# Optimization experiments

Hardware: AMD Instinct MI355X
Metric: run time of the kernel (lower is better)

Reference implementation:

```python
import jax, jax.numpy as jnp
import numpy as np
from jax import lax

SEGMENTS = 64
KERNEL = 5


def setup_inputs() -> dict:
    key = jax.random.key(0)
    k1, k2, k3 = jax.random.split(key, 3)
    B, S, F = 4, 4096, 1024
    A6 = 512 * 6
    inp = jax.random.normal(k1, (B, S, F), dtype=jnp.float32)
    W = jax.random.normal(k2, (A6, F), dtype=jnp.float32) * (1.0 / np.sqrt(F))
    b = jax.random.normal(k3, (A6,), dtype=jnp.float32) * 0.01
    return {"inp": inp, "W": W, "b": b}


def reference(inp, W, b):
    # Fused projection: [B,S,F] @ [F,6A] -> [B,S,6A]
    x = jnp.einsum('bsf,af->bsa', inp, W) + b
    qry, key, val, seg, loc, out = jnp.split(x, 6, axis=2)  # each [B,S,A]
    B, S, A = out.shape

    # Global aggregated attention branch
    agg = qry.mean(axis=1)                              # [B,A]
    scores = jnp.einsum('ba,bsa->bs', agg, key)         # [B,S]
    w = jax.nn.softmax(scores, axis=1)                  # [B,S]
    ctx = jnp.einsum('bs,bsa->ba', w, val)              # [B,A]
    aggregated = ctx[:, None, :] * out                  # [B,S,A]

    # Segment max-pool branch
    nseg = S // SEGMENTS
    seg4 = seg.reshape(B, nseg, SEGMENTS, A)
    seg_max = seg4.max(axis=2, keepdims=True)           # [B,nseg,1,A]
    segment_max_pooled = (seg_max * out.reshape(B, nseg, SEGMENTS, A)).reshape(B, S, A)

    # Local sliding-window max-pool branch (stride 1, pad KERNEL//2, -inf padding)
    pad = KERNEL // 2
    local_max_pooled = lax.reduce_window(
        loc, -jnp.inf, lax.max,
        window_dimensions=(1, KERNEL, 1),
        window_strides=(1, 1, 1),
        padding=((0, 0), (pad, pad), (0, 0)))           # [B,S,A]

    return aggregated + segment_max_pooled + local_max_pooled
```

## Files before the change

kernel.cpp:

```cpp
#include <hip/hip_runtime.h>
#include <hip/hip_bf16.h>
#include <stdint.h>

#define B_    4
#define S_    4096
#define F_    1024
#define A_    512
#define N3_   1536
#define M_    16384

#define BM    256
#define BK    64
#define NT    (F_ / BK)
#define LDP   266

typedef __attribute__((ext_vector_type(8))) __bf16 bf16x8;

#define MFMA(a, b, c) __builtin_amdgcn_mfma_f32_16x16x32_bf16((a), (b), (c), 0, 0, 0)
typedef __attribute__((ext_vector_type(4))) float f32x4;

__device__ __forceinline__ float bflo(unsigned int u) {
  union { unsigned int i; float f; } v; v.i = u << 16; return v.f;
}
__device__ __forceinline__ float bfhi(unsigned int u) {
  union { unsigned int i; float f; } v; v.i = u & 0xffff0000u; return v.f;
}
__device__ __forceinline__ float bf1(unsigned short u) {
  union { unsigned int i; float f; } v; v.i = ((unsigned int)u) << 16; return v.f;
}
__device__ __forceinline__ unsigned short bfc(float f) {
  return __builtin_bit_cast(unsigned short, __float2bfloat16(f));
}
__device__ __forceinline__ ushort4 cvt_bf4(float4 v) {
  ushort4 o;
  o.x = bfc(v.x); o.y = bfc(v.y); o.z = bfc(v.z); o.w = bfc(v.w);
  return o;
}

typedef __attribute__((address_space(3))) unsigned int lds_uint;
typedef const __attribute__((address_space(1))) unsigned int glob_uint;
__device__ __forceinline__ void lds_load16(const void* g, void* l) {
  __builtin_amdgcn_global_load_lds((glob_uint*)g, (lds_uint*)l, 16, 0, 0);
}

__global__ __launch_bounds__(256) void convert_mean_kernel(
    const float* __restrict__ inp, const float* __restrict__ W,
    unsigned short* __restrict__ inp_bf, unsigned short* __restrict__ w_bf,
    float* __restrict__ mu) {
  int blk = blockIdx.x;
  int t   = threadIdx.x;
  int r0  = blk * 32;
  int b   = r0 >> 12;
  float acc0 = 0.f, acc1 = 0.f, acc2 = 0.f, acc3 = 0.f;
  for (int r = 0; r < 32; r++) {
    size_t row = (size_t)(r0 + r);
    float4 v = ((const float4*)(inp + row * F_))[t];
    acc0 += v.x; acc1 += v.y; acc2 += v.z; acc3 += v.w;
    ((ushort4*)(inp_bf + row * F_))[t] = cvt_bf4(v);
  }
  atomicAdd(&mu[b * F_ + t * 4 + 0], acc0);
  atomicAdd(&mu[b * F_ + t * 4 + 1], acc1);
  atomicAdd(&mu[b * F_ + t * 4 + 2], acc2);
  atomicAdd(&mu[b * F_ + t * 4 + 3], acc3);

  const float* Wc = W + (size_t)N3_ * F_;
  const int n4 = (N3_ * F_) / 4;
  for (int i = blk * 256 + t; i < n4; i += 512 * 256) {
    ((ushort4*)w_bf)[i] = cvt_bf4(((const float4*)Wc)[i]);
  }
}

__global__ void agg_kernel(const float* __restrict__ mu, const float* __restrict__ W,
                           const float* __restrict__ bias, float* __restrict__ agg) {
  int gw = blockIdx.x * 4 + (threadIdx.x >> 6);
  int lane = threadIdx.x & 63;
  int b = gw >> 9, a = gw & 511;
  const float4* wr = (const float4*)(W + (size_t)a * F_);
  const float4* mr = (const float4*)(mu + b * F_);
  float s = 0.f;
#pragma unroll
  for (int k = 0; k < 4; k++) {
    float4 wv = wr[lane + 64 * k], mv = mr[lane + 64 * k];
    s += wv.x * mv.x + wv.y * mv.y + wv.z * mv.z + wv.w * mv.w;
  }
  for (int off = 32; off; off >>= 1) s += __shfl_down(s, off);
  if (lane == 0) agg[b * A_ + a] = s * (1.f / S_) + bias[a];
}

__global__ void v_kernel(const float* __restrict__ agg, const float* __restrict__ W,
                         float* __restrict__ v) {
  int fc = blockIdx.x;
  int ac = blockIdx.y;
  int t = threadIdx.x;
  int f = fc * 256 + t;
  const float* Wk = W + (size_t)A_ * F_;
  float s0 = 0.f, s1 = 0.f, s2 = 0.f, s3 = 0.f;
  int a0 = ac * 64;
  for (int a = a0; a < a0 + 64; a++) {
    float wv = Wk[(size_t)a * F_ + f];
    s0 += agg[a] * wv;
    s1 += agg[A_ + a] * wv;
    s2 += agg[2 * A_ + a] * wv;
    s3 += agg[3 * A_ + a] * wv;
  }
  atomicAdd(&v[f], s0);
  atomicAdd(&v[F_ + f], s1);
  atomicAdd(&v[2 * F_ + f], s2);
  atomicAdd(&v[3 * F_ + f], s3);
}

__global__ __launch_bounds__(256) void scores_u_kernel(
    const unsigned short* __restrict__ inp_bf, const float* __restrict__ v,
    float* __restrict__ uP, float* __restrict__ mlzl) {
  int blk = blockIdx.x;
  int b = blk >> 6, ch = blk & 63;
  int s0 = ch * 64;
  int t = threadIdx.x, lane = t & 63, wv = t >> 6;
  __shared__ float sc[64];
  __shared__ float wsl[64];

  const float4* vp = (const float4*)(v + b * F_);
  float4 va0 = vp[lane * 2], va1 = vp[lane * 2 + 1];
  float4 vb0 = vp[(lane + 64) * 2], vb1 = vp[(lane + 64) * 2 + 1];
#pragma unroll
  for (int i = 0; i < 16; i++) {
    int r = wv * 16 + i;
    const uint4* ip = (const uint4*)(inp_bf + ((size_t)(b * S_ + s0 + r)) * F_);
    uint4 x0 = ip[lane], x1 = ip[lane + 64];
    float s = bflo(x0.x) * va0.x + bfhi(x0.x) * va0.y + bflo(x0.y) * va0.z + bfhi(x0.y) * va0.w +
              bflo(x0.z) * va1.x + bfhi(x0.z) * va1.y + bflo(x0.w) * va1.z + bfhi(x0.w) * va1.w +
              bflo(x1.x) * vb0.x + bfhi(x1.x) * vb0.y + bflo(x1.y) * vb0.z + bfhi(x1.y) * vb0.w +
              bflo(x1.z) * vb1.x + bfhi(x1.z) * vb1.y + bflo(x1.w) * vb1.z + bfhi(x1.w) * vb1.w;
    for (int off = 32; off; off >>= 1) s += __shfl_down(s, off);
    if (lane == 0) sc[r] = s;
  }
  __syncthreads();

  float m = -1e30f;
#pragma unroll
  for (int i = 0; i < 64; i++) m = fmaxf(m, sc[i]);
  if (t < 64) wsl[t] = __expf(sc[t] - m);
  __syncthreads();

  {
    const unsigned short* xp = inp_bf + ((size_t)(b * S_ + s0)) * F_ + t * 4;
    float a0 = 0.f, a1 = 0.f, a2 = 0.f, a3 = 0.f;
    for (int s = 0; s < 64; s++) {
      uint2 xv = *(const uint2*)&xp[(size_t)s * F_];
      float w = wsl[s];
      a0 += w * bflo(xv.x); a1 += w * bfhi(xv.x);
      a2 += w * bflo(xv.y); a3 += w * bfhi(xv.y);
    }
    float4 o; o.x = a0; o.y = a1; o.z = a2; o.w = a3;
    *(float4*)&uP[(size_t)blk * 1024 + t * 4] = o;
  }
  if (t == 0) {
    float Z = 0.f;
#pragma unroll
    for (int i = 0; i < 64; i++) Z += wsl[i];
    mlzl[blk * 2] = m; mlzl[blk * 2 + 1] = Z;
  }
}

__global__ void ufin_kernel(const float* __restrict__ uP, const float* __restrict__ mlzl,
                            float* __restrict__ u) {
  int b = blockIdx.x >> 2, fs = blockIdx.x & 3;
  int f = fs * 256 + threadIdx.x;
  float M = -1e30f;
#pragma unroll
  for (int i = 0; i < 64; i++) M = fmaxf(M, mlzl[(b * 64 + i) * 2]);
  float Z = 0.f;
#pragma unroll
  for (int i = 0; i < 64; i++) Z += __expf(mlzl[(b * 64 + i) * 2] - M) * mlzl[(b * 64 + i) * 2 + 1];
  float acc = 0.f;
  for (int ch = 0; ch < 64; ch++) {
    float sc = __expf(mlzl[(b * 64 + ch) * 2] - M);
    acc += sc * uP[(size_t)(b * 64 + ch) * 1024 + f];
  }
  u[b * F_ + f] = acc / Z;
}

__global__ void ctx_kernel(const float* __restrict__ u, const float* __restrict__ W,
                           const float* __restrict__ bias, float* __restrict__ ctx) {
  int gw = blockIdx.x * 4 + (threadIdx.x >> 6);
  int lane = threadIdx.x & 63;
  int b = gw >> 9, a = gw & 511;
  const float4* wr = (const float4*)(W + (size_t)(2 * A_ + a) * F_);
  const float4* ur = (const float4*)(u + b * F_);
  float s = 0.f;
#pragma unroll
  for (int k = 0; k < 4; k++) {
    float4 wv = wr[lane + 64 * k], uv = ur[lane + 64 * k];
    s += wv.x * uv.x + wv.y * uv.y + wv.z * uv.z + wv.w * uv.w;
  }
  for (int off = 32; off; off >>= 1) s += __shfl_down(s, off);
  if (lane == 0) ctx[b * A_ + a] = s + bias[2 * A_ + a];
}

__global__ __launch_bounds__(512, 2) void gemm_fused(
    const __hip_bfloat16* __restrict__ Abf,
    const __hip_bfloat16* __restrict__ Wbf,
    const float* __restrict__ biasP,
    const float* __restrict__ ctx,
    float* __restrict__ out,
    unsigned short* __restrict__ sideLoc,
    float* __restrict__ sideGO) {
  extern __shared__ unsigned short smem[];
  unsigned short* ldsA = smem;
  unsigned short* ldsB = smem + 32768;
  unsigned short* Xt   = smem;
  float* segred = (float*)((char*)smem + 192 * LDP * 2);

  int bid = blockIdx.x;
  int swz = (bid & 7) * 64 + (bid >> 3);
  int mb = swz >> 3;
  int nb = swz & 7;

  int tid  = threadIdx.x;
  int lane = tid & 63;
  int wv   = tid >> 6;
  int wm   = wv >> 1;
  int wn   = wv & 1;
  int lo   = lane & 15, hi = lane >> 4, sw = lane & 7;

  int bir0 = (((hi * 16)      ^ (sw << 4)) >> 1);
  int bir1 = (((64 + hi * 16) ^ (sw << 4)) >> 1);

  const __hip_bfloat16* Ab = Abf + (size_t)mb * BM * F_;

  int srow = tid >> 3;
  int sel  = ((tid & 7) ^ (srow & 7)) * 8;
  int ldst = wv * 512;

  f32x4 acc[4][6];
#pragma unroll
  for (int i = 0; i < 4; i++)
#pragma unroll
    for (int j = 0; j < 6; j++) acc[i][j] = (f32x4){0.f, 0.f, 0.f, 0.f};

  int aBase = (wm * 64 + lo) * 64;
  int bBase = (wn * 96 + lo) * 64;

#define STG_A(kt_, buf_, r_)                                                              \
  lds_load16(Ab + (size_t)((r_) * 64 + srow) * F_ + (kt_) * BK + sel,                     \
             ldsA + (buf_) * 16384 + (r_) * 4096 + ldst)
#define STG_B(kt_, buf_, q_)                                                              \
  lds_load16(Wbf + (size_t)((q_) * 512 + nb * 64 + srow) * F_ + (kt_) * BK + sel,         \
             ldsB + (buf_) * 12288 + (q_) * 4096 + ldst)

  bf16x8 af[4][2], b01[2][2], b23[2][2], b45[2][2];

  STG_A(0, 0, 0); STG_A(0, 0, 1); STG_A(0, 0, 2); STG_A(0, 0, 3);
  STG_B(0, 0, 0); STG_B(0, 0, 1); STG_B(0, 0, 2);
  asm volatile("s_waitcnt vmcnt(0)" ::: "memory");
  __builtin_amdgcn_s_barrier();
#pragma unroll
  for (int i = 0; i < 4; i++) {
    af[i][0] = *(const bf16x8*)&ldsA[aBase + i * 1024 + bir0];
    af[i][1] = *(const bf16x8*)&ldsA[aBase + i * 1024 + bir1];
  }
#pragma unroll
  for (int j = 0; j < 2; j++) {
    b01[j][0] = *(const bf16x8*)&ldsB[bBase + j * 1024 + bir0];
    b01[j][1] = *(const bf16x8*)&ldsB[bBase + j * 1024 + bir1];
  }

  for (int kt = 0; kt < NT; ++kt) {
    int c = kt & 1, nx = c ^ 1;
    bool pf = (kt + 1 < NT);
    const unsigned short* lb  = ldsB + c * 12288;
    const unsigned short* lan = ldsA + nx * 16384;
    const unsigned short* lbn = ldsB + nx * 12288;

    if (pf) { STG_A(kt + 1, nx, 0); STG_A(kt + 1, nx, 1); STG_A(kt + 1, nx, 2); STG_A(kt + 1, nx, 3); }
    asm volatile("s_waitcnt lgkmcnt(0)" ::: "memory");
    __builtin_amdgcn_sched_barrier(0);
    __builtin_amdgcn_s_setprio(1);
#pragma unroll
    for (int i = 0; i < 4; i++)
#pragma unroll
      for (int j = 0; j < 2; j++) {
        acc[i][j] = MFMA(af[i][0], b01[j][0], acc[i][j]);
        acc[i][j] = MFMA(af[i][1], b01[j][1], acc[i][j]);
      }
    __builtin_amdgcn_s_setprio(0);
#pragma unroll
    for (int j = 0; j < 2; j++) {
      b23[j][0] = *(const bf16x8*)&lb[bBase + (2 + j) * 1024 + bir0];
      b23[j][1] = *(const bf16x8*)&lb[bBase + (2 + j) * 1024 + bir1];
    }
    __builtin_amdgcn_s_barrier();

    if (pf) { STG_B(kt + 1, nx, 0); STG_B(kt + 1, nx, 1); STG_B(kt + 1, nx, 2); }
    asm volatile("s_waitcnt lgkmcnt(0)" ::: "memory");
    __builtin_amdgcn_sched_barrier(0);
    __builtin_amdgcn_s_setprio(1);
#pragma unroll
    for (int i = 0; i < 4; i++)
#pragma unroll
      for (int j = 0; j < 2; j++) {
        acc[i][2 + j] = MFMA(af[i][0], b23[j][0], acc[i][2 + j]);
        acc[i][2 + j] = MFMA(af[i][1], b23[j][1], acc[i][2 + j]);
      }
    __builtin_amdgcn_s_setprio(0);
#pragma unroll
    for (int j = 0; j < 2; j++) {
      b45[j][0] = *(const bf16x8*)&lb[bBase + (4 + j) * 1024 + bir0];
      b45[j][1] = *(const bf16x8*)&lb[bBase + (4 + j) * 1024 + bir1];
    }
    __builtin_amdgcn_s_barrier();

    asm volatile("s_waitcnt lgkmcnt(0)" ::: "memory");
    __builtin_amdgcn_sched_barrier(0);
    __builtin_amdgcn_s_setprio(1);
#pragma unroll
    for (int i = 0; i < 4; i++)
#pragma unroll
      for (int j = 0; j < 2; j++) {
        acc[i][4 + j] = MFMA(af[i][0], b45[j][0], acc[i][4 + j]);
        acc[i][4 + j] = MFMA(af[i][1], b45[j][1], acc[i][4 + j]);
      }
    __builtin_amdgcn_s_setprio(0);
    if (pf) asm volatile("s_waitcnt vmcnt(0)" ::: "memory");
    __builtin_amdgcn_s_barrier();
    if (pf) {
#pragma unroll
      for (int i = 0; i < 4; i++) {
        af[i][0] = *(const bf16x8*)&lan[aBase + i * 1024 + bir0];
        af[i][1] = *(const bf16x8*)&lan[aBase + i * 1024 + bir1];
      }
#pragma unroll
      for (int j = 0; j < 2; j++) {
        b01[j][0] = *(const bf16x8*)&lbn[bBase + j * 1024 + bir0];
        b01[j][1] = *(const bf16x8*)&lbn[bBase + j * 1024 + bir1];
      }
    }
  }
#undef STG_A
#undef STG_B

  float bias_r[6];
#pragma unroll
  for (int fj = 0; fj < 6; fj++) {
    int cl = wn * 96 + fj * 16 + lo;
    bias_r[fj] = biasP[(cl >> 6) * 512 + nb * 64 + (cl & 63)];
  }
#pragma unroll
  for (int fi = 0; fi < 4; fi++) {
#pragma unroll
    for (int fj = 0; fj < 6; fj++) {
      int cl = wn * 96 + fj * 16 + lo;
      int r  = wm * 64 + fi * 16 + hi * 4;
      float v0 = acc[fi][fj][0] + bias_r[fj];
      float v1 = acc[fi][fj][1] + bias_r[fj];
      float v2 = acc[fi][fj][2] + bias_r[fj];
      float v3 = acc[fi][fj][3] + bias_r[fj];
      unsigned int u01 = (unsigned int)bfc(v0) | ((unsigned int)bfc(v1) << 16);
      unsigned int u23 = (unsigned int)bfc(v2) | ((unsigned int)bfc(v3) << 16);
      *(unsigned int*)&Xt[cl * LDP + r]     = u01;
      *(unsigned int*)&Xt[cl * LDP + r + 2] = u23;
    }
  }
  __syncthreads();

  if (tid < 256) {
    int seg = tid >> 6, c = tid & 63;
    int base = c * LDP + seg * 64;
    float m = -1e30f;
#pragma unroll
    for (int k = 0; k < 32; k++) {
      unsigned int uu = *(const unsigned int*)&Xt[base + 2 * k];
      m = fmaxf(m, fmaxf(bflo(uu), bfhi(uu)));
    }
    segred[seg * 64 + c] = m;
  }
  __syncthreads();

  {
    int c  = lane;
    int r0 = wv * 32;
    int b  = mb >> 4;
    int gcol = nb * 64 + c;
    float g = ctx[b * 512 + gcol] + segred[(r0 >> 6) * 64 + c];
    int lbase = (64 + c) * LDP;
    int obase = (128 + c) * LDP;
    float lw0 = bf1(Xt[lbase + max(r0 - 2, 0)]);
    float lw1 = bf1(Xt[lbase + max(r0 - 1, 0)]);
    float lw2 = bf1(Xt[lbase + r0]);
    float lw3 = bf1(Xt[lbase + r0 + 1]);
    size_t obase_g = ((size_t)(mb * 256 + r0)) * 512 + gcol;
#pragma unroll
    for (int j = 0; j < 32; j++) {
      int rn = min(r0 + j + 2, 255);
      float lw4 = bf1(Xt[lbase + rn]);
      float lm = fmaxf(fmaxf(fmaxf(lw0, lw1), fmaxf(lw2, lw3)), lw4);
      float o = bf1(Xt[obase + r0 + j]);
      out[obase_g + (size_t)j * 512] = g * o + lm;
      lw0 = lw1; lw1 = lw2; lw2 = lw3; lw3 = lw4;
    }
  }

  if (tid < 256) {
    int rsel = tid >> 6, c = tid & 63;
    int r = (rsel < 2) ? rsel : (252 + rsel);
    int b = mb >> 4;
    float g = ctx[b * 512 + nb * 64 + c] + segred[(r >> 6) * 64 + c];
    float o = bf1(Xt[(128 + c) * LDP + r]);
    int gr = mb * 4 + rsel;
    sideLoc[gr * 512 + nb * 64 + c] = Xt[(64 + c) * LDP + r];
    sideGO[gr * 512 + nb * 64 + c]  = g * o;
  }
}

__global__ void fixup_kernel(const unsigned short* __restrict__ sideLoc,
                             const float* __restrict__ sideGO,
                             float* __restrict__ out) {
  int rb = blockIdx.x;
  int tb = rb & 15;
  int t = threadIdx.x;
  int rsel = t >> 6, cq = t & 63;
#pragma unroll
  for (int k = 0; k < 8; k++) {
    int c = cq * 8 + k;
    float miss;
    int rl;
    if (rsel == 0) {
      if (tb == 0) continue;
      miss = fmaxf(bf1(sideLoc[((rb - 1) * 4 + 2) * 512 + c]),
                   bf1(sideLoc[((rb - 1) * 4 + 3) * 512 + c]));
      rl = 0;
    } else if (rsel == 1) {
      if (tb == 0) continue;
      miss = bf1(sideLoc[((rb - 1) * 4 + 3) * 512 + c]);
      rl = 1;
    } else if (rsel == 2) {
      if (tb == 15) continue;
      miss = bf1(sideLoc[((rb + 1) * 4 + 0) * 512 + c]);
      rl = 254;
    } else {
      if (tb == 15) continue;
      miss = fmaxf(bf1(sideLoc[((rb + 1) * 4 + 0) * 512 + c]),
                   bf1(sideLoc[((rb + 1) * 4 + 1) * 512 + c]));
      rl = 255;
    }
    size_t oi = ((size_t)rb * 256 + rl) * 512 + c;
    float cand = sideGO[(rb * 4 + rsel) * 512 + c] + miss;
    out[oi] = fmaxf(out[oi], cand);
  }
}

extern "C" void kernel_launch(void* const* d_in, const int* in_sizes, int n_in,
                              void* d_out, int out_size, void* d_ws, size_t ws_size,
                              hipStream_t stream) {
  const float* inp  = (const float*)d_in[0];
  const float* W    = (const float*)d_in[1];
  const float* bias = (const float*)d_in[2];
  float* out = (float*)d_out;
  char* ws = (char*)d_ws;

  const size_t INP_OFF  = 0;
  const size_t W_OFF    = 33554432;
  const size_t MU_OFF   = 36700160;
  const size_t U_OFF    = MU_OFF + 16384;
  const size_t V_OFF    = U_OFF + 16384;
  const size_t AGG_OFF  = V_OFF + 16384;
  const size_t CTX_OFF  = AGG_OFF + 8192;
  const size_t SL_OFF   = CTX_OFF + 8192;
  const size_t SG_OFF   = SL_OFF + 262144;
  const size_t UP_OFF   = SG_OFF + 524288;
  const size_t ML_OFF   = UP_OFF + 1048576;

  unsigned short* inp_bf = (unsigned short*)(ws + INP_OFF);
  unsigned short* w_bf   = (unsigned short*)(ws + W_OFF);
  float* mu     = (float*)(ws + MU_OFF);
  float* u      = (float*)(ws + U_OFF);
  float* v      = (float*)(ws + V_OFF);
  float* agg    = (float*)(ws + AGG_OFF);
  float* ctx    = (float*)(ws + CTX_OFF);
  unsigned short* sideLoc = (unsigned short*)(ws + SL_OFF);
  float* sideGO = (float*)(ws + SG_OFF);
  float* uP     = (float*)(ws + UP_OFF);
  float* mlzl   = (float*)(ws + ML_OFF);

  hipFuncSetAttribute(reinterpret_cast<const void*>(gemm_fused),
                      hipFuncAttributeMaxDynamicSharedMemorySize, 114688);

  hipMemsetAsync(ws + MU_OFF, 0, 3 * 16384, stream);
  convert_mean_kernel<<<512, 256, 0, stream>>>(inp, W, inp_bf, w_bf, mu);
  agg_kernel<<<512, 256, 0, stream>>>(mu, W, bias, agg);
  v_kernel<<<dim3(4, 8), 256, 0, stream>>>(agg, W, v);
  scores_u_kernel<<<256, 256, 0, stream>>>(inp_bf, v, uP, mlzl);
  ufin_kernel<<<16, 256, 0, stream>>>(uP, mlzl, u);
  ctx_kernel<<<512, 256, 0, stream>>>(u, W, bias, ctx);
  gemm_fused<<<512, 512, 114688, stream>>>((const __hip_bfloat16*)inp_bf,
                                           (const __hip_bfloat16*)w_bf,
                                           bias + 3 * A_, ctx, out, sideLoc, sideGO);
  fixup_kernel<<<64, 256, 0, stream>>>(sideLoc, sideGO, out);
}
```

Baseline: 128.2 us.

## Restructure GEMM main loop to issue all next-tile loads up front with partial vmcnt wait

Changes the double-buffered GEMM K-loop so that each iteration first issues all global-to-LDS loads for the next A and B tiles. It then waits with vmcnt(7) so only the current tile's loads must be complete, and reads the fragments from the current buffer. The old schedule interleaved A and B prefetch with barriers between MFMA phases and preloaded the next fragments at the end of each iteration. The aim is fewer barriers per iteration and longer overlap of global loads with MFMA work. In exchange, the per-iteration LDS fragment loads now sit on the critical path before the first MFMA group, and the explicit lgkmcnt waits and sched_barriers are gone.

```diff
diff --git a/kernel.cpp b/kernel.cpp
--- a/kernel.cpp
+++ b/kernel.cpp
@@ -15,9 +15,9 @@
 #define LDP   266
 
 typedef __attribute__((ext_vector_type(8))) __bf16 bf16x8;
+typedef __attribute__((ext_vector_type(4))) float f32x4;
 
 #define MFMA(a, b, c) __builtin_amdgcn_mfma_f32_16x16x32_bf16((a), (b), (c), 0, 0, 0)
-typedef __attribute__((ext_vector_type(4))) float f32x4;
 
 __device__ __forceinline__ float bflo(unsigned int u) {
   union { unsigned int i; float f; } v; v.i = u << 16; return v.f;
@@ -248,33 +248,36 @@
   lds_load16(Wbf + (size_t)((q_) * 512 + nb * 64 + srow) * F_ + (kt_) * BK + sel,         \
              ldsB + (buf_) * 12288 + (q_) * 4096 + ldst)
 
-  bf16x8 af[4][2], b01[2][2], b23[2][2], b45[2][2];
-
   STG_A(0, 0, 0); STG_A(0, 0, 1); STG_A(0, 0, 2); STG_A(0, 0, 3);
   STG_B(0, 0, 0); STG_B(0, 0, 1); STG_B(0, 0, 2);
-  asm volatile("s_waitcnt vmcnt(0)" ::: "memory");
-  __builtin_amdgcn_s_barrier();
-#pragma unroll
-  for (int i = 0; i < 4; i++) {
-    af[i][0] = *(const bf16x8*)&ldsA[aBase + i * 1024 + bir0];
-    af[i][1] = *(const bf16x8*)&ldsA[aBase + i * 1024 + bir1];
-  }
-#pragma unroll
-  for (int j = 0; j < 2; j++) {
-    b01[j][0] = *(const bf16x8*)&ldsB[bBase + j * 1024 + bir0];
-    b01[j][1] = *(const bf16x8*)&ldsB[bBase + j * 1024 + bir1];
-  }
 
   for (int kt = 0; kt < NT; ++kt) {
     int c = kt & 1, nx = c ^ 1;
     bool pf = (kt + 1 < NT);
-    const unsigned short* lb  = ldsB + c * 12288;
-    const unsigned short* lan = ldsA + nx * 16384;
-    const unsigned short* lbn = ldsB + nx * 12288;
-
-    if (pf) { STG_A(kt + 1, nx, 0); STG_A(kt + 1, nx, 1); STG_A(kt + 1, nx, 2); STG_A(kt + 1, nx, 3); }
-    asm volatile("s_waitcnt lgkmcnt(0)" ::: "memory");
-    __builtin_amdgcn_sched_barrier(0);
+    const unsigned short* la = ldsA + c * 16384;
+    const unsigned short* lb = ldsB + c * 12288;
+
+    __builtin_amdgcn_s_barrier();
+    if (pf) {
+      STG_A(kt + 1, nx, 0); STG_A(kt + 1, nx, 1); STG_A(kt + 1, nx, 2); STG_A(kt + 1, nx, 3);
+      STG_B(kt + 1, nx, 0); STG_B(kt + 1, nx, 1); STG_B(kt + 1, nx, 2);
+      asm volatile("s_waitcnt vmcnt(7)" ::: "memory");
+    } else {
+      asm volatile("s_waitcnt vmcnt(0)" ::: "memory");
+    }
+    __builtin_amdgcn_s_barrier();
+
+    bf16x8 af[4][2], b01[2][2], b23[2][2], b45[2][2];
+#pragma unroll
+    for (int i = 0; i < 4; i++) {
+      af[i][0] = *(const bf16x8*)&la[aBase + i * 1024 + bir0];
+      af[i][1] = *(const bf16x8*)&la[aBase + i * 1024 + bir1];
+    }
+#pragma unroll
+    for (int j = 0; j < 2; j++) {
+      b01[j][0] = *(const bf16x8*)&lb[bBase + j * 1024 + bir0];
+      b01[j][1] = *(const bf16x8*)&lb[bBase + j * 1024 + bir1];
+    }
     __builtin_amdgcn_s_setprio(1);
 #pragma unroll
     for (int i = 0; i < 4; i++)
@@ -284,16 +287,12 @@
         acc[i][j] = MFMA(af[i][1], b01[j][1], acc[i][j]);
       }
     __builtin_amdgcn_s_setprio(0);
+
 #pragma unroll
     for (int j = 0; j < 2; j++) {
       b23[j][0] = *(const bf16x8*)&lb[bBase + (2 + j) * 1024 + bir0];
       b23[j][1] = *(const bf16x8*)&lb[bBase + (2 + j) * 1024 + bir1];
     }
-    __builtin_amdgcn_s_barrier();
-
-    if (pf) { STG_B(kt + 1, nx, 0); STG_B(kt + 1, nx, 1); STG_B(kt + 1, nx, 2); }
-    asm volatile("s_waitcnt lgkmcnt(0)" ::: "memory");
-    __builtin_amdgcn_sched_barrier(0);
     __builtin_amdgcn_s_setprio(1);
 #pragma unroll
     for (int i = 0; i < 4; i++)
@@ -303,15 +302,12 @@
         acc[i][2 + j] = MFMA(af[i][1], b23[j][1], acc[i][2 + j]);
       }
     __builtin_amdgcn_s_setprio(0);
+
 #pragma unroll
     for (int j = 0; j < 2; j++) {
       b45[j][0] = *(const bf16x8*)&lb[bBase + (4 + j) * 1024 + bir0];
       b45[j][1] = *(const bf16x8*)&lb[bBase + (4 + j) * 1024 + bir1];
     }
-    __builtin_amdgcn_s_barrier();
-
-    asm volatile("s_waitcnt lgkmcnt(0)" ::: "memory");
-    __builtin_amdgcn_sched_barrier(0);
     __builtin_amdgcn_s_setprio(1);
 #pragma unroll
     for (int i = 0; i < 4; i++)
@@ -321,23 +317,11 @@
         acc[i][4 + j] = MFMA(af[i][1], b45[j][1], acc[i][4 + j]);
       }
     __builtin_amdgcn_s_setprio(0);
-    if (pf) asm volatile("s_waitcnt vmcnt(0)" ::: "memory");
-    __builtin_amdgcn_s_barrier();
-    if (pf) {
-#pragma unroll
-      for (int i = 0; i < 4; i++) {
-        af[i][0] = *(const bf16x8*)&lan[aBase + i * 1024 + bir0];
-        af[i][1] = *(const bf16x8*)&lan[aBase + i * 1024 + bir1];
-      }
-#pragma unroll
-      for (int j = 0; j < 2; j++) {
-        b01[j][0] = *(const bf16x8*)&lbn[bBase + j * 1024 + bir0];
-        b01[j][1] = *(const bf16x8*)&lbn[bBase + j * 1024 + bir1];
-      }
-    }
   }
 #undef STG_A
 #undef STG_B
+
+  __syncthreads();
 
   float bias_r[6];
 #pragma unroll
```

Result: no change. 129.4 us (+1.0%).
